# Kernel tuning notes

Measured on AMD Instinct MI355X. Metric: run time of the kernel, lower is better.

The kernel has to match this reference:

```python
import jax, jax.numpy as jnp
import numpy as np

ROLLBACK = 1  # rollback_range: warp at 2**rollback finer resolution, then downsample
B, C, H, W = 2, 32, 512, 512
CIN = 3 * (C // 2) + 2  # inner module input channels


def _bilinear_warp(img, res):
    """Bilinear gather. img: [B,Cc,Hh,Ww]; res: [B,Hh,Ww,2] pixel offsets (x,y).
    Samples img at (x+res_x, y+res_y) with zero padding outside."""
    Bb, Cc, Hh, Ww = img.shape
    gy, gx = jnp.meshgrid(jnp.arange(Hh, dtype=img.dtype),
                          jnp.arange(Ww, dtype=img.dtype), indexing='ij')
    sx = gx[None] + res[..., 0]  # [B,Hh,Ww]
    sy = gy[None] + res[..., 1]
    x0 = jnp.floor(sx); y0 = jnp.floor(sy)
    wx = sx - x0; wy = sy - y0

    def gather(yi, xi):
        inb = ((yi >= 0) & (yi < Hh) & (xi >= 0) & (xi < Ww)).astype(img.dtype)
        yc = jnp.clip(yi, 0, Hh - 1).astype(jnp.int32)
        xc = jnp.clip(xi, 0, Ww - 1).astype(jnp.int32)
        v = jax.vmap(lambda im, y, x: im[:, y, x])(img, yc, xc)  # [B,Cc,Hh,Ww]
        return v * inb[:, None]

    v00 = gather(y0, x0);     v01 = gather(y0, x0 + 1)
    v10 = gather(y0 + 1, x0); v11 = gather(y0 + 1, x0 + 1)
    wx = wx[:, None]; wy = wy[:, None]  # broadcast over channels
    return (v00 * (1 - wy) * (1 - wx) + v01 * (1 - wy) * wx
            + v10 * wy * (1 - wx) + v11 * wy * wx)


def _resize_img(img, f):  # [B,Cc,Hh,Ww] bilinear spatial resize
    Bb, Cc, Hh, Ww = img.shape
    return jax.image.resize(img, (Bb, Cc, int(Hh * f), int(Ww * f)), 'bilinear')


def _resize_res(res, f):  # [B,Hh,Ww,2]; pixel-unit values scale with resolution
    Bb, Hh, Ww, _ = res.shape
    return jax.image.resize(res, (Bb, int(Hh * f), int(Ww * f), 2), 'bilinear') * f


def res_warp_img(img, res, rollback):
    if rollback > 0:
        f = 2 ** rollback
        out = _bilinear_warp(_resize_img(img, f), _resize_res(res, f))
        return _resize_img(out, 1.0 / f)
    return _bilinear_warp(img, res)


def res_warp_res(res_a, res_b, rollback):
    # warp residual field a (treated as a 2-channel image, values in pixel units) by b
    if rollback > 0:
        f = 2 ** rollback
        a = _resize_res(res_a, f); b = _resize_res(res_b, f)
        out = jnp.transpose(_bilinear_warp(jnp.transpose(a, (0, 3, 1, 2)), b), (0, 2, 3, 1))
        return _resize_res(out, 1.0 / f)
    out = _bilinear_warp(jnp.transpose(res_a, (0, 3, 1, 2)), res_b)
    return jnp.transpose(out, (0, 2, 3, 1))


def combine_residuals(res_a, res_b, rollback):
    # flow composition: apply a then b
    return res_b + res_warp_res(res_a, res_b, rollback)


def _conv3x3(x, w, b):
    y = jax.lax.conv_general_dilated(x, w, (1, 1), 'SAME',
                                     dimension_numbers=('NCHW', 'OIHW', 'NCHW'))
    return y + b[None, :, None, None]


def setup_inputs() -> dict:
    key = jax.random.key(0)
    k1, k2, k3 = jax.random.split(key, 3)
    x = jax.random.normal(k1, (B, C, H, W), dtype=jnp.float32)
    res = jax.random.normal(k2, (B, 2, H, W), dtype=jnp.float32)  # ~1px flow
    W_inner = jax.random.normal(k3, (2, CIN, 3, 3), dtype=jnp.float32) * 0.02
    b_inner = jnp.zeros((2,), dtype=jnp.float32)
    return {"x": x, "res": res, "W_inner": W_inner, "b_inner": b_inner, "level": 0}


def reference(x, res, W_inner, b_inner, level):
    res_hw = jnp.transpose(res, (0, 2, 3, 1))  # [B,H,W,2]
    nf = x.shape[1]
    src, tgt = x[:, :nf // 2], x[:, nf // 2:]
    warped_tgt = res_warp_img(tgt, res_hw, ROLLBACK)
    bundle = jnp.concatenate([src, tgt, warped_tgt, res], axis=1)  # [B,3C/2+2,H,W]
    adj = _conv3x3(bundle, W_inner, b_inner)  # hindsight_adjustment [B,2,H,W]
    # mode == 'combine_res': state['down'][level]['input'] = combined residual
    new_res = combine_residuals(res_hw, jnp.transpose(adj, (0, 2, 3, 1)), ROLLBACK)
    hindsight_warped_tgt = res_warp_img(tgt, new_res, ROLLBACK)
    return jnp.concatenate([src, hindsight_warped_tgt], axis=1)  # [B,C,H,W]
```

## Files before the change

### kernel.cpp

```cpp
#include <hip/hip_runtime.h>
#include <hip/hip_bf16.h>
#include <cstdint>
#include <cstddef>

#define HW   512
#define HW2  1024
#define SZ   (512 * 512)
#define NPT  (34 * 34)
#define K_PTS 5
#define SRCW 36
#define NSRC (SRCW * SRCW)
#define MARG 9

struct UpTap { int i0, i1; float w0, w1; };

__device__ __forceinline__ UpTap up_tap(int i) {
  UpTap t;
  int k = i >> 1;
  if ((i & 1) == 0) {
    t.i0 = k - 1; t.i1 = k; t.w0 = 0.25f; t.w1 = 0.75f;
    if (k == 0) { t.i0 = 0; t.w0 = 0.0f; t.w1 = 1.0f; }
  } else {
    t.i0 = k; t.i1 = k + 1; t.w0 = 0.75f; t.w1 = 0.25f;
    if (k == HW - 1) { t.i1 = HW - 1; t.w0 = 1.0f; t.w1 = 0.0f; }
  }
  return t;
}

__device__ __forceinline__ float up_at(const float* __restrict__ plane, int yi, int xi) {
  UpTap ty = up_tap(yi), tx = up_tap(xi);
  const float* r0 = plane + (size_t)ty.i0 * HW;
  const float* r1 = plane + (size_t)ty.i1 * HW;
  float v00 = r0[tx.i0], v01 = r0[tx.i1];
  float v10 = r1[tx.i0], v11 = r1[tx.i1];
  return ty.w0 * (tx.w0 * v00 + tx.w1 * v01) + ty.w1 * (tx.w0 * v10 + tx.w1 * v11);
}

__device__ __forceinline__ void axis_taps(float s, int& base, float& w0, float& w1, float& w2) {
  float f0 = floorf(s);
  int i0 = (int)f0;
  float fr = s - f0;
  int b = (i0 & 1) ? (i0 >> 1) : (i0 >> 1) - 1;
  b = b < 0 ? 0 : (b > (HW - 3) ? (HW - 3) : b);
  float w[3] = {0.0f, 0.0f, 0.0f};
  if ((unsigned)i0 < (unsigned)HW2) {
    UpTap t = up_tap(i0);
    w[t.i0 - b] += (1.0f - fr) * t.w0;
    w[t.i1 - b] += (1.0f - fr) * t.w1;
  }
  if ((unsigned)(i0 + 1) < (unsigned)HW2) {
    UpTap t = up_tap(i0 + 1);
    w[t.i0 - b] += fr * t.w0;
    w[t.i1 - b] += fr * t.w1;
  }
  base = b; w0 = w[0]; w1 = w[1]; w2 = w[2];
}

__global__ void copy_src_kernel(const float* __restrict__ x, float* __restrict__ out) {
  const size_t half = (size_t)16 * SZ;
  const size_t nvec = half / 4;
  size_t i = (size_t)blockIdx.x * blockDim.x + threadIdx.x;
  if (i < 2 * nvec) {
    size_t b = i / nvec, j = i % nvec;
    const float4* s = (const float4*)(x + b * 2 * half);
    float4* d = (float4*)(out + b * 2 * half);
    d[j] = s[j];
  }
}

struct PtTaps {
  int   locoff;
  float wy0, wy1, wy2, wx0, wx1, wx2;
};

__device__ __forceinline__ void compute_taps(const float* __restrict__ fx,
                                             const float* __restrict__ fy,
                                             int gx0, int gy0, int xo, int yo, int tid,
                                             PtTaps (&pt)[K_PTS]) {
  #pragma unroll
  for (int i = 0; i < K_PTS; ++i) {
    int p = tid + i * 256;
    pt[i].locoff = 0;
    pt[i].wy0 = pt[i].wy1 = pt[i].wy2 = 0.0f;
    pt[i].wx0 = pt[i].wx1 = pt[i].wx2 = 0.0f;
    if (p < NPT) {
      int ry = p / 34, rx = p % 34;
      int yy = gy0 + ry, xx = gx0 + rx;
      if ((unsigned)yy < (unsigned)HW2 && (unsigned)xx < (unsigned)HW2) {
        float sx = (float)xx + 2.0f * up_at(fx, yy, xx);
        float sy = (float)yy + 2.0f * up_at(fy, yy, xx);
        int bx, by;
        axis_taps(sx, bx, pt[i].wx0, pt[i].wx1, pt[i].wx2);
        axis_taps(sy, by, pt[i].wy0, pt[i].wy1, pt[i].wy2);
        int rx_ = bx - xo, ry_ = by - yo;
        if ((unsigned)rx_ <= (unsigned)(SRCW - 3) && (unsigned)ry_ <= (unsigned)(SRCW - 3))
          pt[i].locoff = ry_ * SRCW + rx_;
        else
          pt[i].locoff = ~(by * HW + bx);
      }
    }
  }
}

__device__ __forceinline__ void stage_pair(const float* __restrict__ p0,
                                           const float* __restrict__ p1,
                                           float2* __restrict__ s_src,
                                           int xo, int yo, int tid) {
  #pragma unroll
  for (int i = 0; i < 6; ++i) {
    int p = tid + i * 256;
    if (p < NSRC) {
      int r = p / SRCW, c = p % SRCW;
      int gy = yo + r; gy = gy < 0 ? 0 : (gy > HW - 1 ? HW - 1 : gy);
      int gx = xo + c; gx = gx < 0 ? 0 : (gx > HW - 1 ? HW - 1 : gx);
      size_t o = (size_t)gy * HW + gx;
      s_src[p] = make_float2(p0[o], p1[o]);
    }
  }
}

__device__ __forceinline__ float eval3_global(const float* __restrict__ pl, int off, const PtTaps& t) {
  const float* p0 = pl + off;
  float r0 = t.wx0 * p0[0]        + t.wx1 * p0[1]          + t.wx2 * p0[2];
  float r1 = t.wx0 * p0[HW]       + t.wx1 * p0[HW + 1]     + t.wx2 * p0[HW + 2];
  float r2 = t.wx0 * p0[2 * HW]   + t.wx1 * p0[2 * HW + 1] + t.wx2 * p0[2 * HW + 2];
  return t.wy0 * r0 + t.wy1 * r1 + t.wy2 * r2;
}

__device__ __forceinline__ void eval_round(const float2* __restrict__ s_src,
                                           float2* __restrict__ s_tile,
                                           const float* __restrict__ plane0,
                                           const float* __restrict__ plane1,
                                           const PtTaps (&pt)[K_PTS], int tid) {
  #pragma unroll
  for (int i = 0; i < K_PTS; ++i) {
    int p = tid + i * 256;
    if (p < NPT) {
      const PtTaps t = pt[i];
      float a0, a1;
      if (t.locoff >= 0) {
        const float2* s = s_src + t.locoff;
        float2 v00 = s[0],        v01 = s[1],            v02 = s[2];
        float2 v10 = s[SRCW],     v11 = s[SRCW + 1],     v12 = s[SRCW + 2];
        float2 v20 = s[2 * SRCW], v21 = s[2 * SRCW + 1], v22 = s[2 * SRCW + 2];
        float r00 = t.wx0 * v00.x + t.wx1 * v01.x + t.wx2 * v02.x;
        float r10 = t.wx0 * v10.x + t.wx1 * v11.x + t.wx2 * v12.x;
        float r20 = t.wx0 * v20.x + t.wx1 * v21.x + t.wx2 * v22.x;
        float r01 = t.wx0 * v00.y + t.wx1 * v01.y + t.wx2 * v02.y;
        float r11 = t.wx0 * v10.y + t.wx1 * v11.y + t.wx2 * v12.y;
        float r21 = t.wx0 * v20.y + t.wx1 * v21.y + t.wx2 * v22.y;
        a0 = t.wy0 * r00 + t.wy1 * r10 + t.wy2 * r20;
        a1 = t.wy0 * r01 + t.wy1 * r11 + t.wy2 * r21;
      } else {
        int off = ~t.locoff;
        a0 = eval3_global(plane0, off, t);
        a1 = eval3_global(plane1, off, t);
      }
      s_tile[p] = make_float2(a0, a1);
    }
  }
}

__global__ void warp_img_kernel(const float* __restrict__ x,
                                const float* __restrict__ res,
                                float* __restrict__ out)
{
  __shared__ float2 s_src[NSRC];
  __shared__ float2 s_tile[NPT];

  const int b = blockIdx.z;
  const int tx0 = blockIdx.x * 16, ty0 = blockIdx.y * 16;
  const int gx0 = tx0 * 2 - 1, gy0 = ty0 * 2 - 1;
  const int xo = tx0 - MARG, yo = ty0 - MARG;
  const int tid = threadIdx.x;

  const float* resx = res + (size_t)b * 2 * SZ;
  const float* resy = resx + SZ;
  const float* tgt  = x + ((size_t)b * 32 + 16) * SZ;

  stage_pair(tgt, tgt + SZ, s_src, xo, yo, tid);

  PtTaps pt[K_PTS];
  compute_taps(resx, resy, gx0, gy0, xo, yo, tid, pt);

  const int ly = tid >> 4, lx = tid & 15;
  const int oy = ty0 + ly, ox = tx0 + lx;
  const float RW[4] = {0.25f, 0.75f, 0.75f, 0.25f};
  float wy[4], wx[4];
  float sumy = 0.f, sumx = 0.f;
  #pragma unroll
  for (int d = 0; d < 4; ++d) {
    int g = 2 * oy - 1 + d;
    wy[d] = ((unsigned)g < (unsigned)HW2) ? RW[d] : 0.0f; sumy += wy[d];
    g = 2 * ox - 1 + d;
    wx[d] = ((unsigned)g < (unsigned)HW2) ? RW[d] : 0.0f; sumx += wx[d];
  }
  const float inv = 1.0f / (sumy * sumx);

  __syncthreads();

  for (int c = 0; c < 16; c += 2) {
    const float* plane0 = tgt + (size_t)c * SZ;
    eval_round(s_src, s_tile, plane0, plane0 + SZ, pt, tid);
    __syncthreads();

    if (c < 14)
      stage_pair(plane0 + 2 * SZ, plane0 + 3 * SZ, s_src, xo, yo, tid);

    float acc0 = 0.0f, acc1 = 0.0f;
    #pragma unroll
    for (int dy = 0; dy < 4; ++dy) {
      float r0 = 0.0f, r1 = 0.0f;
      const int base = (2 * ly + dy) * 34 + 2 * lx;
      #pragma unroll
      for (int dx = 0; dx < 4; ++dx) {
        float2 v = s_tile[base + dx];
        r0 += wx[dx] * v.x;
        r1 += wx[dx] * v.y;
      }
      acc0 += wy[dy] * r0;
      acc1 += wy[dy] * r1;
    }
    size_t o = (((size_t)b * 32 + 16 + c) * HW + oy) * HW + ox;
    out[o] = acc0 * inv;
    out[o + SZ] = acc1 * inv;
    __syncthreads();
  }
}

__global__ void conv_kernel(const float* __restrict__ x,
                            const float* __restrict__ warped,
                            const float* __restrict__ res,
                            const float* __restrict__ Wc,
                            const float* __restrict__ bc,
                            float* __restrict__ adj)
{
  __shared__ float sw[900];
  const int tid = threadIdx.y * 16 + threadIdx.x;
  for (int i = tid; i < 900; i += 256) sw[i] = Wc[i];
  __syncthreads();

  const int b = blockIdx.z;
  const int oy = blockIdx.y * 16 + threadIdx.y;
  const int ox = blockIdx.x * 16 + threadIdx.x;

  float acc0 = bc[0];
  float acc1 = bc[1];

  for (int ic = 0; ic < 50; ++ic) {
    const float* w0 = &sw[ic * 9];
    const float* w1 = &sw[450 + ic * 9];
    const float* plane;
    if (ic < 32)      plane = x      + ((size_t)b * 32 + ic) * SZ;
    else if (ic < 48) plane = warped + ((size_t)b * 32 + 16 + (ic - 32)) * SZ;
    else              plane = res    + ((size_t)b * 2 + (ic - 48)) * SZ;
    #pragma unroll
    for (int ky = 0; ky < 3; ++ky) {
      int yy = oy + ky - 1;
      bool yok = (unsigned)yy < (unsigned)HW;
      #pragma unroll
      for (int kx = 0; kx < 3; ++kx) {
        int xx = ox + kx - 1;
        float v = 0.0f;
        if (yok && (unsigned)xx < (unsigned)HW)
          v = plane[(size_t)yy * HW + xx];
        acc0 += v * w0[ky * 3 + kx];
        acc1 += v * w1[ky * 3 + kx];
      }
    }
  }
  adj[((size_t)b * 2 + 0) * SZ + (size_t)oy * HW + ox] = acc0;
  adj[((size_t)b * 2 + 1) * SZ + (size_t)oy * HW + ox] = acc1;
}

__global__ void new_res_kernel(const float* __restrict__ res,
                               const float* __restrict__ adj,
                               float* __restrict__ nres)
{
  __shared__ float2 s_src[NSRC];
  __shared__ float2 s_tile[NPT];

  const int b = blockIdx.z;
  const int tx0 = blockIdx.x * 16, ty0 = blockIdx.y * 16;
  const int gx0 = tx0 * 2 - 1, gy0 = ty0 * 2 - 1;
  const int xo = tx0 - MARG, yo = ty0 - MARG;
  const int tid = threadIdx.x;

  const float* adjx = adj + (size_t)b * 2 * SZ;
  const float* adjy = adjx + SZ;
  const float* res0 = res + (size_t)b * 2 * SZ;
  const float* res1 = res0 + SZ;

  stage_pair(res0, res1, s_src, xo, yo, tid);

  PtTaps pt[K_PTS];
  compute_taps(adjx, adjy, gx0, gy0, xo, yo, tid, pt);

  const int ly = tid >> 4, lx = tid & 15;
  const int oy = ty0 + ly, ox = tx0 + lx;
  const float RW[4] = {0.25f, 0.75f, 0.75f, 0.25f};
  float wy[4], wx[4];
  float sumy = 0.f, sumx = 0.f;
  #pragma unroll
  for (int d = 0; d < 4; ++d) {
    int g = 2 * oy - 1 + d;
    wy[d] = ((unsigned)g < (unsigned)HW2) ? RW[d] : 0.0f; sumy += wy[d];
    g = 2 * ox - 1 + d;
    wx[d] = ((unsigned)g < (unsigned)HW2) ? RW[d] : 0.0f; sumx += wx[d];
  }
  const float inv = 1.0f / (sumy * sumx);

  __syncthreads();
  eval_round(s_src, s_tile, res0, res1, pt, tid);
  __syncthreads();

  float acc0 = 0.0f, acc1 = 0.0f;
  #pragma unroll
  for (int dy = 0; dy < 4; ++dy) {
    float r0 = 0.0f, r1 = 0.0f;
    const int base = (2 * ly + dy) * 34 + 2 * lx;
    #pragma unroll
    for (int dx = 0; dx < 4; ++dx) {
      float2 v = s_tile[base + dx];
      r0 += wx[dx] * v.x;
      r1 += wx[dx] * v.y;
    }
    acc0 += wy[dy] * r0;
    acc1 += wy[dy] * r1;
  }
  size_t o = ((size_t)b * 2) * SZ + (size_t)oy * HW + ox;
  nres[o]      = acc0 * inv + adjx[(size_t)oy * HW + ox];
  nres[o + SZ] = acc1 * inv + adjy[(size_t)oy * HW + ox];
}

extern "C" void kernel_launch(void* const* d_in, const int* in_sizes, int n_in,
                              void* d_out, int out_size, void* d_ws, size_t ws_size,
                              hipStream_t stream) {
  const float* x   = (const float*)d_in[0];
  const float* res = (const float*)d_in[1];
  const float* Wc  = (const float*)d_in[2];
  const float* bc  = (const float*)d_in[3];
  float* out = (float*)d_out;

  float* adj  = (float*)d_ws;
  float* nres = adj + (size_t)2 * 2 * SZ;

  {
    const size_t nvec = 2 * ((size_t)16 * SZ / 4);
    copy_src_kernel<<<dim3((unsigned)((nvec + 255) / 256)), dim3(256), 0, stream>>>(x, out);
  }

  dim3 tile_grid(32, 32, 2);

  warp_img_kernel<<<tile_grid, dim3(256), 0, stream>>>(x, res, out);

  conv_kernel<<<tile_grid, dim3(16, 16), 0, stream>>>(x, out, res, Wc, bc, adj);

  new_res_kernel<<<tile_grid, dim3(256), 0, stream>>>(res, adj, nres);

  warp_img_kernel<<<tile_grid, dim3(256), 0, stream>>>(x, nres, out);
}
```

Baseline: 411.7 us.

## Stage conv halos in double-buffered LDS and split warp tiles into padded planes

The 3x3 conv now loads each input channel's 18x18 halo tile into shared memory, double-buffered, with the next channel prefetched into registers while the current one is computed. This replaces nine bounds-checked global loads per pixel per channel. The warp kernels switch from interleaved float2 shared tiles to separate float planes with a padded row stride of 37, to cut LDS bank conflicts, and add launch bounds that ask for higher occupancy. The cost is more barriers in the conv loop, plus register pressure from the launch-bound hint.

After: 775.3 us. 1.88x slower.

```diff
diff --git a/kernel.cpp b/kernel.cpp
--- a/kernel.cpp
+++ b/kernel.cpp
@@ -9,6 +9,7 @@
 #define NPT  (34 * 34)
 #define K_PTS 5
 #define SRCW 36
+#define SRCP 37
 #define NSRC (SRCW * SRCW)
 #define MARG 9
 
@@ -94,7 +95,7 @@
         axis_taps(sy, by, pt[i].wy0, pt[i].wy1, pt[i].wy2);
         int rx_ = bx - xo, ry_ = by - yo;
         if ((unsigned)rx_ <= (unsigned)(SRCW - 3) && (unsigned)ry_ <= (unsigned)(SRCW - 3))
-          pt[i].locoff = ry_ * SRCW + rx_;
+          pt[i].locoff = ry_ * SRCP + rx_;
         else
           pt[i].locoff = ~(by * HW + bx);
       }
@@ -104,7 +105,8 @@
 
 __device__ __forceinline__ void stage_pair(const float* __restrict__ p0,
                                            const float* __restrict__ p1,
-                                           float2* __restrict__ s_src,
+                                           float* __restrict__ s0,
+                                           float* __restrict__ s1,
                                            int xo, int yo, int tid) {
   #pragma unroll
   for (int i = 0; i < 6; ++i) {
@@ -114,7 +116,9 @@
       int gy = yo + r; gy = gy < 0 ? 0 : (gy > HW - 1 ? HW - 1 : gy);
       int gx = xo + c; gx = gx < 0 ? 0 : (gx > HW - 1 ? HW - 1 : gx);
       size_t o = (size_t)gy * HW + gx;
-      s_src[p] = make_float2(p0[o], p1[o]);
+      int d = r * SRCP + c;
+      s0[d] = p0[o];
+      s1[d] = p1[o];
     }
   }
 }
@@ -127,8 +131,10 @@
   return t.wy0 * r0 + t.wy1 * r1 + t.wy2 * r2;
 }
 
-__device__ __forceinline__ void eval_round(const float2* __restrict__ s_src,
-                                           float2* __restrict__ s_tile,
+__device__ __forceinline__ void eval_round(const float* __restrict__ s0,
+                                           const float* __restrict__ s1,
+                                           float* __restrict__ t0,
+                                           float* __restrict__ t1,
                                            const float* __restrict__ plane0,
                                            const float* __restrict__ plane1,
                                            const PtTaps (&pt)[K_PTS], int tid) {
@@ -139,16 +145,14 @@
       const PtTaps t = pt[i];
       float a0, a1;
       if (t.locoff >= 0) {
-        const float2* s = s_src + t.locoff;
-        float2 v00 = s[0],        v01 = s[1],            v02 = s[2];
-        float2 v10 = s[SRCW],     v11 = s[SRCW + 1],     v12 = s[SRCW + 2];
-        float2 v20 = s[2 * SRCW], v21 = s[2 * SRCW + 1], v22 = s[2 * SRCW + 2];
-        float r00 = t.wx0 * v00.x + t.wx1 * v01.x + t.wx2 * v02.x;
-        float r10 = t.wx0 * v10.x + t.wx1 * v11.x + t.wx2 * v12.x;
-        float r20 = t.wx0 * v20.x + t.wx1 * v21.x + t.wx2 * v22.x;
-        float r01 = t.wx0 * v00.y + t.wx1 * v01.y + t.wx2 * v02.y;
-        float r11 = t.wx0 * v10.y + t.wx1 * v11.y + t.wx2 * v12.y;
-        float r21 = t.wx0 * v20.y + t.wx1 * v21.y + t.wx2 * v22.y;
+        const float* a = s0 + t.locoff;
+        const float* b = s1 + t.locoff;
+        float r00 = t.wx0 * a[0]        + t.wx1 * a[1]            + t.wx2 * a[2];
+        float r10 = t.wx0 * a[SRCP]     + t.wx1 * a[SRCP + 1]     + t.wx2 * a[SRCP + 2];
+        float r20 = t.wx0 * a[2 * SRCP] + t.wx1 * a[2 * SRCP + 1] + t.wx2 * a[2 * SRCP + 2];
+        float r01 = t.wx0 * b[0]        + t.wx1 * b[1]            + t.wx2 * b[2];
+        float r11 = t.wx0 * b[SRCP]     + t.wx1 * b[SRCP + 1]     + t.wx2 * b[SRCP + 2];
+        float r21 = t.wx0 * b[2 * SRCP] + t.wx1 * b[2 * SRCP + 1] + t.wx2 * b[2 * SRCP + 2];
         a0 = t.wy0 * r00 + t.wy1 * r10 + t.wy2 * r20;
         a1 = t.wy0 * r01 + t.wy1 * r11 + t.wy2 * r21;
       } else {
@@ -156,17 +160,21 @@
         a0 = eval3_global(plane0, off, t);
         a1 = eval3_global(plane1, off, t);
       }
-      s_tile[p] = make_float2(a0, a1);
-    }
-  }
-}
-
-__global__ void warp_img_kernel(const float* __restrict__ x,
-                                const float* __restrict__ res,
-                                float* __restrict__ out)
+      t0[p] = a0;
+      t1[p] = a1;
+    }
+  }
+}
+
+__global__ void __launch_bounds__(256, 8)
+warp_img_kernel(const float* __restrict__ x,
+                const float* __restrict__ res,
+                float* __restrict__ out)
 {
-  __shared__ float2 s_src[NSRC];
-  __shared__ float2 s_tile[NPT];
+  __shared__ float s_src0[36 * SRCP];
+  __shared__ float s_src1[36 * SRCP];
+  __shared__ float s_tile0[NPT];
+  __shared__ float s_tile1[NPT];
 
   const int b = blockIdx.z;
   const int tx0 = blockIdx.x * 16, ty0 = blockIdx.y * 16;
@@ -178,7 +186,7 @@
   const float* resy = resx + SZ;
   const float* tgt  = x + ((size_t)b * 32 + 16) * SZ;
 
-  stage_pair(tgt, tgt + SZ, s_src, xo, yo, tid);
+  stage_pair(tgt, tgt + SZ, s_src0, s_src1, xo, yo, tid);
 
   PtTaps pt[K_PTS];
   compute_taps(resx, resy, gx0, gy0, xo, yo, tid, pt);
@@ -201,11 +209,11 @@
 
   for (int c = 0; c < 16; c += 2) {
     const float* plane0 = tgt + (size_t)c * SZ;
-    eval_round(s_src, s_tile, plane0, plane0 + SZ, pt, tid);
+    eval_round(s_src0, s_src1, s_tile0, s_tile1, plane0, plane0 + SZ, pt, tid);
     __syncthreads();
 
     if (c < 14)
-      stage_pair(plane0 + 2 * SZ, plane0 + 3 * SZ, s_src, xo, yo, tid);
+      stage_pair(plane0 + 2 * SZ, plane0 + 3 * SZ, s_src0, s_src1, xo, yo, tid);
 
     float acc0 = 0.0f, acc1 = 0.0f;
     #pragma unroll
@@ -214,9 +222,8 @@
       const int base = (2 * ly + dy) * 34 + 2 * lx;
       #pragma unroll
       for (int dx = 0; dx < 4; ++dx) {
-        float2 v = s_tile[base + dx];
-        r0 += wx[dx] * v.x;
-        r1 += wx[dx] * v.y;
+        r0 += wx[dx] * s_tile0[base + dx];
+        r1 += wx[dx] * s_tile1[base + dx];
       }
       acc0 += wy[dy] * r0;
       acc1 += wy[dy] * r1;
@@ -228,57 +235,108 @@
   }
 }
 
-__global__ void conv_kernel(const float* __restrict__ x,
-                            const float* __restrict__ warped,
-                            const float* __restrict__ res,
-                            const float* __restrict__ Wc,
-                            const float* __restrict__ bc,
-                            float* __restrict__ adj)
+#define CHN 18
+#define CHE (CHN * CHN)
+
+__global__ void __launch_bounds__(256)
+conv_kernel(const float* __restrict__ x,
+            const float* __restrict__ warped,
+            const float* __restrict__ res,
+            const float* __restrict__ Wc,
+            const float* __restrict__ bc,
+            float* __restrict__ adj)
 {
   __shared__ float sw[900];
-  const int tid = threadIdx.y * 16 + threadIdx.x;
+  __shared__ float sh[2][CHE];
+
+  const int tid = threadIdx.x;
   for (int i = tid; i < 900; i += 256) sw[i] = Wc[i];
-  __syncthreads();
 
   const int b = blockIdx.z;
-  const int oy = blockIdx.y * 16 + threadIdx.y;
-  const int ox = blockIdx.x * 16 + threadIdx.x;
+  const int tx0 = blockIdx.x * 16, ty0 = blockIdx.y * 16;
+  const int ty = tid >> 4, tx = tid & 15;
 
   float acc0 = bc[0];
   float acc1 = bc[1];
 
+  const float* px = x + (size_t)b * 32 * SZ;
+  const float* pw = warped + ((size_t)b * 32 + 16) * SZ;
+  const float* pr = res + (size_t)b * 2 * SZ;
+
+  #define PLANE(ic) ((ic) < 32 ? px + (size_t)(ic) * SZ \
+                   : (ic) < 48 ? pw + (size_t)((ic) - 32) * SZ \
+                   : pr + (size_t)((ic) - 48) * SZ)
+
+  float rb0, rb1;
+  {
+    const float* pl = PLANE(0);
+    rb0 = 0.f; rb1 = 0.f;
+    int p = tid;
+    { int ry = p / CHN, rx = p % CHN;
+      int gy = ty0 - 1 + ry, gx = tx0 - 1 + rx;
+      if ((unsigned)gy < (unsigned)HW && (unsigned)gx < (unsigned)HW) rb0 = pl[(size_t)gy * HW + gx]; }
+    p = tid + 256;
+    if (p < CHE) {
+      int ry = p / CHN, rx = p % CHN;
+      int gy = ty0 - 1 + ry, gx = tx0 - 1 + rx;
+      if ((unsigned)gy < (unsigned)HW && (unsigned)gx < (unsigned)HW) rb1 = pl[(size_t)gy * HW + gx];
+    }
+    sh[0][tid] = rb0;
+    if (tid + 256 < CHE) sh[0][tid + 256] = rb1;
+  }
+
   for (int ic = 0; ic < 50; ++ic) {
+    __syncthreads();
+    if (ic < 49) {
+      const float* pl = PLANE(ic + 1);
+      rb0 = 0.f; rb1 = 0.f;
+      int p = tid;
+      { int ry = p / CHN, rx = p % CHN;
+        int gy = ty0 - 1 + ry, gx = tx0 - 1 + rx;
+        if ((unsigned)gy < (unsigned)HW && (unsigned)gx < (unsigned)HW) rb0 = pl[(size_t)gy * HW + gx]; }
+      p = tid + 256;
+      if (p < CHE) {
+        int ry = p / CHN, rx = p % CHN;
+        int gy = ty0 - 1 + ry, gx = tx0 - 1 + rx;
+        if ((unsigned)gy < (unsigned)HW && (unsigned)gx < (unsigned)HW) rb1 = pl[(size_t)gy * HW + gx];
+      }
+    }
+
+    const float* hp = sh[ic & 1];
     const float* w0 = &sw[ic * 9];
     const float* w1 = &sw[450 + ic * 9];
-    const float* plane;
-    if (ic < 32)      plane = x      + ((size_t)b * 32 + ic) * SZ;
-    else if (ic < 48) plane = warped + ((size_t)b * 32 + 16 + (ic - 32)) * SZ;
-    else              plane = res    + ((size_t)b * 2 + (ic - 48)) * SZ;
     #pragma unroll
     for (int ky = 0; ky < 3; ++ky) {
-      int yy = oy + ky - 1;
-      bool yok = (unsigned)yy < (unsigned)HW;
       #pragma unroll
       for (int kx = 0; kx < 3; ++kx) {
-        int xx = ox + kx - 1;
-        float v = 0.0f;
-        if (yok && (unsigned)xx < (unsigned)HW)
-          v = plane[(size_t)yy * HW + xx];
+        float v = hp[(ty + ky) * CHN + tx + kx];
         acc0 += v * w0[ky * 3 + kx];
         acc1 += v * w1[ky * 3 + kx];
       }
     }
-  }
+
+    if (ic < 49) {
+      float* sd = sh[(ic + 1) & 1];
+      sd[tid] = rb0;
+      if (tid + 256 < CHE) sd[tid + 256] = rb1;
+    }
+  }
+  #undef PLANE
+
+  const int oy = ty0 + ty, ox = tx0 + tx;
   adj[((size_t)b * 2 + 0) * SZ + (size_t)oy * HW + ox] = acc0;
   adj[((size_t)b * 2 + 1) * SZ + (size_t)oy * HW + ox] = acc1;
 }
 
-__global__ void new_res_kernel(const float* __restrict__ res,
-                               const float* __restrict__ adj,
-                               float* __restrict__ nres)
+__global__ void __launch_bounds__(256, 8)
+new_res_kernel(const float* __restrict__ res,
+               const float* __restrict__ adj,
+               float* __restrict__ nres)
 {
-  __shared__ float2 s_src[NSRC];
-  __shared__ float2 s_tile[NPT];
+  __shared__ float s_src0[36 * SRCP];
+  __shared__ float s_src1[36 * SRCP];
+  __shared__ float s_tile0[NPT];
+  __shared__ float s_tile1[NPT];
 
   const int b = blockIdx.z;
   const int tx0 = blockIdx.x * 16, ty0 = blockIdx.y * 16;
@@ -291,7 +349,7 @@
   const float* res0 = res + (size_t)b * 2 * SZ;
   const float* res1 = res0 + SZ;
 
-  stage_pair(res0, res1, s_src, xo, yo, tid);
+  stage_pair(res0, res1, s_src0, s_src1, xo, yo, tid);
 
   PtTaps pt[K_PTS];
   compute_taps(adjx, adjy, gx0, gy0, xo, yo, tid, pt);
@@ -311,7 +369,7 @@
   const float inv = 1.0f / (sumy * sumx);
 
   __syncthreads();
-  eval_round(s_src, s_tile, res0, res1, pt, tid);
+  eval_round(s_src0, s_src1, s_tile0, s_tile1, res0, res1, pt, tid);
   __syncthreads();
 
   float acc0 = 0.0f, acc1 = 0.0f;
@@ -321,9 +379,8 @@
     const int base = (2 * ly + dy) * 34 + 2 * lx;
     #pragma unroll
     for (int dx = 0; dx < 4; ++dx) {
-      float2 v = s_tile[base + dx];
-      r0 += wx[dx] * v.x;
-      r1 += wx[dx] * v.y;
+      r0 += wx[dx] * s_tile0[base + dx];
+      r1 += wx[dx] * s_tile1[base + dx];
     }
     acc0 += wy[dy] * r0;
     acc1 += wy[dy] * r1;
@@ -354,7 +411,7 @@
 
   warp_img_kernel<<<tile_grid, dim3(256), 0, stream>>>(x, res, out);
 
-  conv_kernel<<<tile_grid, dim3(16, 16), 0, stream>>>(x, out, res, Wc, bc, adj);
+  conv_kernel<<<tile_grid, dim3(256), 0, stream>>>(x, out, res, Wc, bc, adj);
 
   new_res_kernel<<<tile_grid, dim3(256), 0, stream>>>(res, adj, nres);
 
```

## Fuse src copy into conv and stage conv inputs through double-buffered LDS halo tiles

Applied to the files above, without the earlier changes.

Removes the separate copy kernel that wrote the src half of the output and instead writes those channels from the conv kernel, using the center tap it already loads. The conv now loads each 18x18 halo tile of two input channels into shared memory, double-buffered and prefetched one step ahead, rather than issuing nine global loads per channel per thread. This removes a full read and write pass over half of x and cuts redundant global traffic in the conv. In exchange it adds shared-memory use and a barrier per channel pair.

Result: faster. 377.4 us (-8.3%).

```diff
diff --git a/kernel.cpp b/kernel.cpp
--- a/kernel.cpp
+++ b/kernel.cpp
@@ -54,18 +54,6 @@
     w[t.i1 - b] += fr * t.w1;
   }
   base = b; w0 = w[0]; w1 = w[1]; w2 = w[2];
-}
-
-__global__ void copy_src_kernel(const float* __restrict__ x, float* __restrict__ out) {
-  const size_t half = (size_t)16 * SZ;
-  const size_t nvec = half / 4;
-  size_t i = (size_t)blockIdx.x * blockDim.x + threadIdx.x;
-  if (i < 2 * nvec) {
-    size_t b = i / nvec, j = i % nvec;
-    const float4* s = (const float4*)(x + b * 2 * half);
-    float4* d = (float4*)(out + b * 2 * half);
-    d[j] = s[j];
-  }
 }
 
 struct PtTaps {
@@ -228,49 +216,113 @@
   }
 }
 
-__global__ void conv_kernel(const float* __restrict__ x,
-                            const float* __restrict__ warped,
-                            const float* __restrict__ res,
-                            const float* __restrict__ Wc,
-                            const float* __restrict__ bc,
-                            float* __restrict__ adj)
+#define CHN 18
+#define CHE (CHN * CHN)
+
+__global__ void __launch_bounds__(256)
+conv_kernel(const float* __restrict__ x,
+            const float* __restrict__ res,
+            const float* __restrict__ Wc,
+            const float* __restrict__ bc,
+            float* __restrict__ out,
+            float* __restrict__ adj)
 {
   __shared__ float sw[900];
-  const int tid = threadIdx.y * 16 + threadIdx.x;
+  __shared__ float sh[4][CHE];
+
+  const int tid = threadIdx.x;
   for (int i = tid; i < 900; i += 256) sw[i] = Wc[i];
-  __syncthreads();
 
   const int b = blockIdx.z;
-  const int oy = blockIdx.y * 16 + threadIdx.y;
-  const int ox = blockIdx.x * 16 + threadIdx.x;
+  const int tx0 = blockIdx.x * 16, ty0 = blockIdx.y * 16;
+  const int ty = tid >> 4, tx = tid & 15;
+
+  const float* px = x + (size_t)b * 32 * SZ;
+  const float* pw = out + ((size_t)b * 32 + 16) * SZ;
+  const float* pr = res + (size_t)b * 2 * SZ;
+
+  const int ry0 = tid / CHN, rx0 = tid - ry0 * CHN;
+  const int hy0 = ty0 - 1 + ry0, hx0 = tx0 - 1 + rx0;
+  const bool ok0 = (unsigned)hy0 < (unsigned)HW && (unsigned)hx0 < (unsigned)HW;
+  const int off0 = hy0 * HW + hx0;
+  const int p1 = tid + 256;
+  const bool sl1 = p1 < CHE;
+  const int ry1 = p1 / CHN, rx1 = p1 - ry1 * CHN;
+  const int hy1 = ty0 - 1 + ry1, hx1 = tx0 - 1 + rx1;
+  const bool ok1 = sl1 && (unsigned)hy1 < (unsigned)HW && (unsigned)hx1 < (unsigned)HW;
+  const int off1 = hy1 * HW + hx1;
+
+  #define PLANE(ic) ((ic) < 32 ? px + (size_t)(ic) * SZ \
+                   : (ic) < 48 ? pw + (size_t)((ic) - 32) * SZ \
+                   : pr + (size_t)((ic) - 48) * SZ)
 
   float acc0 = bc[0];
   float acc1 = bc[1];
 
-  for (int ic = 0; ic < 50; ++ic) {
-    const float* w0 = &sw[ic * 9];
-    const float* w1 = &sw[450 + ic * 9];
-    const float* plane;
-    if (ic < 32)      plane = x      + ((size_t)b * 32 + ic) * SZ;
-    else if (ic < 48) plane = warped + ((size_t)b * 32 + 16 + (ic - 32)) * SZ;
-    else              plane = res    + ((size_t)b * 2 + (ic - 48)) * SZ;
+  {
+    const float* plE = PLANE(0);
+    const float* plO = PLANE(1);
+    float e0 = ok0 ? plE[off0] : 0.f;
+    float e1 = ok1 ? plE[off1] : 0.f;
+    float o0 = ok0 ? plO[off0] : 0.f;
+    float o1 = ok1 ? plO[off1] : 0.f;
+    sh[0][tid] = e0; if (sl1) sh[0][p1] = e1;
+    sh[1][tid] = o0; if (sl1) sh[1][p1] = o1;
+  }
+
+  const size_t pix = (size_t)(ty0 + ty) * HW + (tx0 + tx);
+
+  for (int kk = 0; kk < 25; ++kk) {
+    __syncthreads();
+    float e0 = 0.f, e1 = 0.f, o0 = 0.f, o1 = 0.f;
+    if (kk < 24) {
+      const float* plE = PLANE(2 * kk + 2);
+      const float* plO = PLANE(2 * kk + 3);
+      e0 = ok0 ? plE[off0] : 0.f;
+      e1 = ok1 ? plE[off1] : 0.f;
+      o0 = ok0 ? plO[off0] : 0.f;
+      o1 = ok1 ? plO[off1] : 0.f;
+    }
+
+    const int cur = (kk & 1) * 2;
+    const float* hpE = sh[cur];
+    const float* hpO = sh[cur + 1];
+    const float* wE0 = &sw[(2 * kk) * 9];
+    const float* wO0 = wE0 + 9;
+    const float* wE1 = &sw[450 + (2 * kk) * 9];
+    const float* wO1 = wE1 + 9;
+    float cE = 0.f, cO = 0.f;
     #pragma unroll
     for (int ky = 0; ky < 3; ++ky) {
-      int yy = oy + ky - 1;
-      bool yok = (unsigned)yy < (unsigned)HW;
       #pragma unroll
       for (int kx = 0; kx < 3; ++kx) {
-        int xx = ox + kx - 1;
-        float v = 0.0f;
-        if (yok && (unsigned)xx < (unsigned)HW)
-          v = plane[(size_t)yy * HW + xx];
-        acc0 += v * w0[ky * 3 + kx];
-        acc1 += v * w1[ky * 3 + kx];
+        float vE = hpE[(ty + ky) * CHN + tx + kx];
+        float vO = hpO[(ty + ky) * CHN + tx + kx];
+        if (ky == 1 && kx == 1) { cE = vE; cO = vO; }
+        acc0 += vE * wE0[ky * 3 + kx];
+        acc0 += vO * wO0[ky * 3 + kx];
+        acc1 += vE * wE1[ky * 3 + kx];
+        acc1 += vO * wO1[ky * 3 + kx];
       }
     }
-  }
-  adj[((size_t)b * 2 + 0) * SZ + (size_t)oy * HW + ox] = acc0;
-  adj[((size_t)b * 2 + 1) * SZ + (size_t)oy * HW + ox] = acc1;
+
+    if (kk < 8) {
+      size_t oc = ((size_t)b * 32 + 2 * kk) * SZ + pix;
+      out[oc] = cE;
+      out[oc + SZ] = cO;
+    }
+
+    if (kk < 24) {
+      float* sE = sh[cur ^ 2];
+      float* sO = sh[(cur ^ 2) + 1];
+      sE[tid] = e0; if (sl1) sE[p1] = e1;
+      sO[tid] = o0; if (sl1) sO[p1] = o1;
+    }
+  }
+  #undef PLANE
+
+  adj[((size_t)b * 2 + 0) * SZ + pix] = acc0;
+  adj[((size_t)b * 2 + 1) * SZ + pix] = acc1;
 }
 
 __global__ void new_res_kernel(const float* __restrict__ res,
@@ -345,16 +397,11 @@
   float* adj  = (float*)d_ws;
   float* nres = adj + (size_t)2 * 2 * SZ;
 
-  {
-    const size_t nvec = 2 * ((size_t)16 * SZ / 4);
-    copy_src_kernel<<<dim3((unsigned)((nvec + 255) / 256)), dim3(256), 0, stream>>>(x, out);
-  }
-
   dim3 tile_grid(32, 32, 2);
 
   warp_img_kernel<<<tile_grid, dim3(256), 0, stream>>>(x, res, out);
 
-  conv_kernel<<<tile_grid, dim3(16, 16), 0, stream>>>(x, out, res, Wc, bc, adj);
+  conv_kernel<<<tile_grid, dim3(256), 0, stream>>>(x, res, Wc, bc, out, adj);
 
   new_res_kernel<<<tile_grid, dim3(256), 0, stream>>>(res, adj, nres);
 
```
